# Kernel tuning notes

Measured on AMD Instinct MI355X. Metric: run time of the kernel, lower is better.

Reference implementation:

```python
import jax, jax.numpy as jnp
import numpy as np

B, N, D, H = 128, 197, 384, 1536  # batch, patches+CLS, embed_dim, hidden_dim


def _layer_norm(x, g, b, eps=1e-5):
    m = jnp.mean(x, axis=-1, keepdims=True)
    v = jnp.mean(jnp.square(x - m), axis=-1, keepdims=True)
    return (x - m) * jax.lax.rsqrt(v + eps) * g + b


def setup_inputs() -> dict:
    key = jax.random.key(0)
    ks = jax.random.split(key, 8)
    x = jax.random.normal(ks[0], (B, N, D), dtype=jnp.float32)
    # quantum circuit surrogates: orthogonal-style square matrices
    V = jax.random.normal(ks[1], (D, D), dtype=jnp.float32) / np.sqrt(D)
    W = jax.random.normal(ks[2], (D, D), dtype=jnp.float32) / np.sqrt(D)
    ln1_g = jnp.ones((D,), jnp.float32); ln1_b = jnp.zeros((D,), jnp.float32)
    ln2_g = jnp.ones((D,), jnp.float32); ln2_b = jnp.zeros((D,), jnp.float32)
    W1 = jax.random.normal(ks[3], (D, H), dtype=jnp.float32) / np.sqrt(D)
    b1 = jnp.zeros((H,), jnp.float32)
    W2 = jax.random.normal(ks[4], (H, D), dtype=jnp.float32) / np.sqrt(H)
    b2 = jnp.zeros((D,), jnp.float32)
    return {"x": x, "ln1_g": ln1_g, "ln1_b": ln1_b, "V": V, "W": W,
            "ln2_g": ln2_g, "ln2_b": ln2_b, "W1": W1, "b1": b1, "W2": W2, "b2": b2}


def reference(x, ln1_g, ln1_b, V, W, ln2_g, ln2_b, W1, b1, W2, b2):
    inp = _layer_norm(x, ln1_g, ln1_b)
    # normalization across the patch axis (dim=1), exactly as in the torch code
    inp = inp / jnp.sqrt(jnp.sum(jnp.square(inp) + 1e-4, axis=1, keepdims=True) + 1e-8)
    # Vx circuit: unary-basis probabilities |(V x_i)_d|^2 -> vx[b, d, i]
    vx = jnp.square(jnp.einsum('de,bne->bdn', V, inp))            # [B, D, N]
    # xWx circuit: (x_i^T W x_j)^2 -> xwx[b, i, j]
    y = jnp.einsum('bnd,de->bne', inp, W)                         # [B, N, D]
    xwx = jnp.square(jnp.einsum('bne,bme->bnm', y, inp))          # [B, N, N]
    vx = jnp.sqrt(vx + 1e-8)
    xwx = jnp.sqrt(xwx + 1e-8)
    attn = jax.nn.softmax(xwx, axis=-1)                           # [B, N, N]
    t = jnp.einsum('bnm,bdm->bnd', attn, vx)                      # attn @ vx^T
    x = x + t
    h = _layer_norm(x, ln2_g, ln2_b)
    h = jax.nn.gelu(h @ W1 + b1) @ W2 + b2                        # dropout=0 (eval)
    return x + h
```

## Files before the change

### kernel.cpp

```cpp
#include <hip/hip_runtime.h>
#include <math.h>

typedef unsigned short u16;
typedef unsigned int u32;
typedef __bf16 bfv8 __attribute__((ext_vector_type(8)));
typedef float f32x4 __attribute__((ext_vector_type(4)));

#define BB 128
#define NN 197
#define DD 384
#define HH 1536
#define BN (BB*NN)
#define NP 224

__device__ __forceinline__ u16 f2bf(float x){ u32 u; __builtin_memcpy(&u,&x,4); u = (u + 0x7fffu + ((u>>16)&1u))>>16; return (u16)u; }

__device__ __forceinline__ float fast_gelu(float z){
  float t2 = 1.5957691216f*z*(1.f + 0.044715f*z*z);
  return z * __builtin_amdgcn_rcpf(1.f + __expf(-t2));
}

__device__ __forceinline__ void gload16(const void* g, void* s){
  __builtin_amdgcn_global_load_lds(
      (const __attribute__((address_space(1))) void*)g,
      (__attribute__((address_space(3))) void*)s, 16, 0, 0);
}

__global__ __launch_bounds__(256) void ln1_stats(const float* __restrict__ x,
    float* __restrict__ mu, float* __restrict__ rv){
  int row = blockIdx.x*4 + (threadIdx.x>>6);
  int lane = threadIdx.x & 63;
  const float* xr = x + (long)row*DD;
  float s=0.f, ss=0.f;
  #pragma unroll
  for (int j=0;j<DD/64;j++){ float v = xr[lane + j*64]; s+=v; ss+=v*v; }
  #pragma unroll
  for (int m=32;m;m>>=1){ s += __shfl_xor(s,m); ss += __shfl_xor(ss,m); }
  if (lane==0){
    float mn = s*(1.f/DD);
    float var = ss*(1.f/DD) - mn*mn;
    mu[row]=mn; rv[row]=1.f/sqrtf(var+1e-5f);
  }
}

__global__ __launch_bounds__(256) void colnorm(const float* __restrict__ x,
    const float* __restrict__ mu, const float* __restrict__ rv,
    const float* __restrict__ g, const float* __restrict__ bt,
    float* __restrict__ scale){
  int i = blockIdx.x*256 + threadIdx.x;
  int b = i/DD, d = i - b*DD;
  const float* xp = x + (long)b*NN*DD + d;
  float gd = g[d], bd = bt[d];
  float s = 0.f;
  for (int n=0;n<NN;n++){
    float v = (xp[(long)n*DD] - mu[b*NN+n]) * rv[b*NN+n] * gd + bd;
    s += v*v;
  }
  scale[i] = 1.f/sqrtf(s + 197.f*1e-4f + 1e-8f);
}

__global__ __launch_bounds__(256) void ln_apply(const float* __restrict__ x,
    const float* __restrict__ mu, const float* __restrict__ rv,
    const float* __restrict__ g, const float* __restrict__ bt,
    const float* __restrict__ scale, u16* __restrict__ inpn){
  long i = (long)blockIdx.x*256 + threadIdx.x;
  int d = (int)(i % DD);
  long row = i / DD;
  int b = (int)(row / NN);
  float v = (x[i]-mu[row])*rv[row]*g[d]+bt[d];
  inpn[i] = f2bf(v * scale[b*DD+d]);
}

__global__ __launch_bounds__(256) void prep_weights(const float* __restrict__ V, const float* __restrict__ W,
    const float* __restrict__ W1, const float* __restrict__ W2,
    u16* __restrict__ Vb, u16* __restrict__ Wt, u16* __restrict__ W1t, u16* __restrict__ W2t){
  int i = blockIdx.x*256 + threadIdx.x;
  if (i < DD*DD){
    Vb[i] = f2bf(V[i]);
    int r = i/DD, c = i - r*DD;
    Wt[c*DD + r] = f2bf(W[i]);
  }
  {
    int r = i/HH, c = i - r*HH;
    W1t[(long)c*DD + r] = f2bf(W1[i]);
    int r2 = i/DD, c2 = i - r2*DD;
    W2t[(long)c2*HH + r2] = f2bf(W2[i]);
  }
}

__global__ __launch_bounds__(256) void softmax_rows(const float* __restrict__ S, u16* __restrict__ attn){
  int row = blockIdx.x*4 + (threadIdx.x>>6);
  int lane = threadIdx.x & 63;
  const float* sr = S + (long)row*NP;
  float v[4]; float mx = -1e30f;
  #pragma unroll
  for (int j=0;j<4;j++){ int c = lane + j*64; v[j] = (c<NN)? sr[c] : -1e30f; mx = fmaxf(mx, v[j]); }
  #pragma unroll
  for (int m=32;m;m>>=1) mx = fmaxf(mx, __shfl_xor(mx,m));
  float sm = 0.f;
  #pragma unroll
  for (int j=0;j<4;j++){ v[j] = __expf(v[j]-mx); sm += v[j]; }
  #pragma unroll
  for (int m=32;m;m>>=1) sm += __shfl_xor(sm,m);
  float inv = __builtin_amdgcn_rcpf(sm);
  u16* ar = attn + (long)row*NP;
  #pragma unroll
  for (int j=0;j<4;j++){ int c = lane + j*64; if (c<NP) ar[c] = f2bf(v[j]*inv); }
}

__global__ __launch_bounds__(256) void ln2_fused(const float* __restrict__ x2,
    const float* __restrict__ g, const float* __restrict__ bt, u16* __restrict__ h){
  int row = blockIdx.x*4 + (threadIdx.x>>6);
  int lane = threadIdx.x & 63;
  const float* xr = x2 + (long)row*DD;
  float v[6]; float s=0.f, ss=0.f;
  #pragma unroll
  for (int j=0;j<6;j++){ v[j]=xr[lane+j*64]; s+=v[j]; ss+=v[j]*v[j]; }
  #pragma unroll
  for (int m=32;m;m>>=1){ s+=__shfl_xor(s,m); ss+=__shfl_xor(ss,m); }
  float mn = s*(1.f/DD);
  float rvv = 1.f/sqrtf(ss*(1.f/DD)-mn*mn+1e-5f);
  u16* hr = h + (long)row*DD;
  #pragma unroll
  for (int j=0;j<6;j++){ int d = lane+j*64; hr[d] = f2bf((v[j]-mn)*rvv*g[d]+bt[d]); }
}

struct EpiUt { u16* ut;
  __device__ void operator()(int, int r0, int c, const f32x4* col) const {
    #pragma unroll
    for (int m=0;m<4;m++)
      #pragma unroll
      for (int i=0;i<4;i++){
        int r = r0 + m*16 + i;
        int b = r/NN, p = r - b*NN;
        float v = col[m][i];
        ut[((long)b*DD + c)*NP + p] = f2bf(sqrtf(v*v + 1e-8f));
      }
  }};
struct EpiY { u16* y;
  __device__ void operator()(int, int r0, int c, const f32x4* col) const {
    u16* yp = y + (long)r0*DD + c;
    #pragma unroll
    for (int m=0;m<4;m++)
      #pragma unroll
      for (int i=0;i<4;i++)
        yp[(long)(m*16+i)*DD] = f2bf(col[m][i]);
  }};
struct EpiS { float* s;
  __device__ void operator()(int b, int r0, int c, const f32x4* col) const {
    float* sp = s + ((long)b*NN + r0)*NP + c;
    #pragma unroll
    for (int m=0;m<4;m++)
      #pragma unroll
      for (int i=0;i<4;i++){
        int r = r0 + m*16 + i;
        float v = col[m][i];
        if (r < NN) sp[(long)(m*16+i)*NP] = sqrtf(v*v + 1e-8f);
      }
  }};
struct EpiX2 { float* x2; const float* x;
  __device__ void operator()(int b, int r0, int c, const f32x4* col) const {
    long base = ((long)b*NN + r0)*DD + c;
    #pragma unroll
    for (int m=0;m<4;m++)
      #pragma unroll
      for (int i=0;i<4;i++){
        int r = r0 + m*16 + i;
        if (r < NN){ long idx = base + (long)(m*16+i)*DD; x2[idx] = x[idx] + col[m][i]; }
      }
  }};
struct EpiGelu { u16* g; const float* b1;
  __device__ void operator()(int, int r0, int c, const f32x4* col) const {
    float bb = b1[c];
    u16* gp = g + (long)r0*HH + c;
    #pragma unroll
    for (int m=0;m<4;m++)
      #pragma unroll
      for (int i=0;i<4;i++)
        gp[(long)(m*16+i)*HH] = f2bf(fast_gelu(col[m][i] + bb));
  }};
struct EpiOut { float* o; const float* x2; const float* b2;
  __device__ void operator()(int, int r0, int c, const f32x4* col) const {
    float bb = b2[c];
    long base = (long)r0*DD + c;
    #pragma unroll
    for (int m=0;m<4;m++)
      #pragma unroll
      for (int i=0;i<4;i++){
        long idx = base + (long)(m*16+i)*DD;
        o[idx] = x2[idx] + col[m][i] + bb;
      }
  }};

template<class Epi>
__global__ __launch_bounds__(256) void gemm_nt(const u16* __restrict__ A, const u16* __restrict__ B,
    int M, int N, int K, int lda, int ldb, long sA, long sB, int NT, Epi epi)
{
  __shared__ __align__(16) u16 As[128*32];
  __shared__ __align__(16) u16 Bs[128*32];
  const int bm = blockIdx.x / NT, bn = blockIdx.x - bm*NT;
  const int bat = blockIdx.y;
  const u16* Ab = A + (long)bat*sA;
  const u16* Bb = B + (long)bat*sB;
  const int t = threadIdx.x, lane = t&63, wid = t>>6, wr = wid>>1, wc = wid&1;
  const int row0 = bm*128, col0 = bn*128;

  long aoff[2], boff[2]; int soff[2];
  #pragma unroll
  for (int i=0;i<2;i++){
    int ob = (i*256+t)*16;
    int r = ob>>6;
    int ke = (ob&63)>>1;
    int ra = row0+r; if (ra>M-1) ra=M-1;
    int rb = col0+r; if (rb>N-1) rb=N-1;
    aoff[i] = (long)ra*lda + ke;
    boff[i] = (long)rb*ldb + ke;
    soff[i] = ob;
  }

  f32x4 acc[4][4] = {};
  const int kg = (lane>>4)*8, rl = lane&15;

  for (int k0=0; k0<K; k0+=32){
    #pragma unroll
    for (int i=0;i<2;i++){
      gload16(Ab + aoff[i] + k0, (char*)As + soff[i]);
      gload16(Bb + boff[i] + k0, (char*)Bs + soff[i]);
    }
    __syncthreads();
    bfv8 af[4], bfr[4];
    #pragma unroll
    for (int m=0;m<4;m++) af[m]  = *(const bfv8*)&As[(wr*64 + m*16 + rl)*32 + kg];
    #pragma unroll
    for (int n=0;n<4;n++) bfr[n] = *(const bfv8*)&Bs[(wc*64 + n*16 + rl)*32 + kg];
    #pragma unroll
    for (int m=0;m<4;m++)
      #pragma unroll
      for (int n=0;n<4;n++)
        acc[m][n] = __builtin_amdgcn_mfma_f32_16x16x32_bf16(af[m], bfr[n], acc[m][n], 0,0,0);
    __syncthreads();
  }

  const int rbase = row0 + wr*64 + (lane>>4)*4;
  const int cbase = col0 + wc*64 + rl;
  #pragma unroll
  for (int n=0;n<4;n++){
    int c = cbase + n*16;
    if (c < N){
      f32x4 colv[4] = {acc[0][n], acc[1][n], acc[2][n], acc[3][n]};
      epi(bat, rbase, c, colv);
    }
  }
}

extern "C" void kernel_launch(void* const* d_in, const int* in_sizes, int n_in,
                              void* d_out, int out_size, void* d_ws, size_t ws_size,
                              hipStream_t stream){
  const float* x     = (const float*)d_in[0];
  const float* g1    = (const float*)d_in[1];
  const float* b1n   = (const float*)d_in[2];
  const float* V     = (const float*)d_in[3];
  const float* W     = (const float*)d_in[4];
  const float* g2    = (const float*)d_in[5];
  const float* b2n   = (const float*)d_in[6];
  const float* W1    = (const float*)d_in[7];
  const float* bias1 = (const float*)d_in[8];
  const float* W2    = (const float*)d_in[9];
  const float* bias2 = (const float*)d_in[10];
  float* out = (float*)d_out;

  char* ws = (char*)d_ws;
  size_t off = 0;
  auto take = [&](size_t bytes)->char*{ char* p = ws + off; off += (bytes + 255) & ~(size_t)255; return p; };

  float* mu    = (float*)take((size_t)BN*4);
  float* rv    = (float*)take((size_t)BN*4);
  float* scale = (float*)take((size_t)BB*DD*4);
  char* aliasBase = ws + off;
  u16*  inpn = (u16*) take((size_t)BN*DD*2);
  u16*  Ut   = (u16*) take((size_t)BB*DD*NP*2);
  u16*  Yb   = (u16*) take((size_t)BN*DD*2);
  float* S   = (float*)take((size_t)BN*NP*4);
  u16*  attn = (u16*) take((size_t)BN*NP*2);
  float* x2  = (float*)take((size_t)BN*DD*4);
  u16*  h    = (u16*) take((size_t)BN*DD*2);
  u16*  Vb   = (u16*) take((size_t)DD*DD*2);
  u16*  Wt   = (u16*) take((size_t)DD*DD*2);
  u16*  W1t  = (u16*) take((size_t)DD*HH*2);
  u16*  W2t  = (u16*) take((size_t)DD*HH*2);
  u16*  G    = (u16*)aliasBase;

  prep_weights<<<DD*HH/256, 256, 0, stream>>>(V, W, W1, W2, Vb, Wt, W1t, W2t);
  ln1_stats  <<<BN/4,       256, 0, stream>>>(x, mu, rv);
  colnorm    <<<BB*DD/256,  256, 0, stream>>>(x, mu, rv, g1, b1n, scale);
  ln_apply   <<<BN*DD/256,  256, 0, stream>>>(x, mu, rv, g1, b1n, scale, inpn);
  (void)hipMemsetAsync(Ut, 0, (size_t)BB*DD*NP*2, stream);

  { dim3 grid(197*3, 1);
    gemm_nt<EpiUt><<<grid,256,0,stream>>>(inpn, Vb, BN, DD, DD, DD, DD, 0, 0, 3, EpiUt{Ut}); }
  { dim3 grid(197*3, 1);
    gemm_nt<EpiY><<<grid,256,0,stream>>>(inpn, Wt, BN, DD, DD, DD, DD, 0, 0, 3, EpiY{Yb}); }
  { dim3 grid(4, BB);
    gemm_nt<EpiS><<<grid,256,0,stream>>>(Yb, inpn, NN, NN, DD, DD, DD,
                                         (long)NN*DD, (long)NN*DD, 2, EpiS{S}); }
  softmax_rows<<<BN/4, 256, 0, stream>>>(S, attn);
  { dim3 grid(6, BB);
    gemm_nt<EpiX2><<<grid,256,0,stream>>>(attn, Ut, NN, DD, NP, NP, NP,
                                          (long)NN*NP, (long)DD*NP, 3, EpiX2{x2, x}); }
  ln2_fused<<<BN/4, 256, 0, stream>>>(x2, g2, b2n, h);
  { dim3 grid(197*12, 1);
    gemm_nt<EpiGelu><<<grid,256,0,stream>>>(h, W1t, BN, HH, DD, DD, DD, 0, 0, 12, EpiGelu{G, bias1}); }
  { dim3 grid(197*3, 1);
    gemm_nt<EpiOut><<<grid,256,0,stream>>>(G, W2t, BN, DD, HH, HH, HH, 0, 0, 3, EpiOut{out, x2, bias2}); }
}
```

Baseline: 442.0 us.

## Fuse LN1 stats, column norm and apply into one per-batch kernel; XCD-aware GEMM tile remap

```diff
diff --git a/kernel.cpp b/kernel.cpp
--- a/kernel.cpp
+++ b/kernel.cpp
@@ -26,49 +26,39 @@
       (__attribute__((address_space(3))) void*)s, 16, 0, 0);
 }
 
-__global__ __launch_bounds__(256) void ln1_stats(const float* __restrict__ x,
-    float* __restrict__ mu, float* __restrict__ rv){
-  int row = blockIdx.x*4 + (threadIdx.x>>6);
-  int lane = threadIdx.x & 63;
-  const float* xr = x + (long)row*DD;
-  float s=0.f, ss=0.f;
-  #pragma unroll
-  for (int j=0;j<DD/64;j++){ float v = xr[lane + j*64]; s+=v; ss+=v*v; }
-  #pragma unroll
-  for (int m=32;m;m>>=1){ s += __shfl_xor(s,m); ss += __shfl_xor(ss,m); }
-  if (lane==0){
-    float mn = s*(1.f/DD);
-    float var = ss*(1.f/DD) - mn*mn;
-    mu[row]=mn; rv[row]=1.f/sqrtf(var+1e-5f);
-  }
-}
-
-__global__ __launch_bounds__(256) void colnorm(const float* __restrict__ x,
-    const float* __restrict__ mu, const float* __restrict__ rv,
-    const float* __restrict__ g, const float* __restrict__ bt,
-    float* __restrict__ scale){
-  int i = blockIdx.x*256 + threadIdx.x;
-  int b = i/DD, d = i - b*DD;
-  const float* xp = x + (long)b*NN*DD + d;
-  float gd = g[d], bd = bt[d];
-  float s = 0.f;
-  for (int n=0;n<NN;n++){
-    float v = (xp[(long)n*DD] - mu[b*NN+n]) * rv[b*NN+n] * gd + bd;
-    s += v*v;
-  }
-  scale[i] = 1.f/sqrtf(s + 197.f*1e-4f + 1e-8f);
-}
-
-__global__ __launch_bounds__(256) void ln_apply(const float* __restrict__ x,
-    const float* __restrict__ mu, const float* __restrict__ rv,
-    const float* __restrict__ g, const float* __restrict__ bt,
-    const float* __restrict__ scale, u16* __restrict__ inpn){
-  long i = (long)blockIdx.x*256 + threadIdx.x;
-  int d = (int)(i % DD);
-  long row = i / DD;
-  int b = (int)(row / NN);
-  float v = (x[i]-mu[row])*rv[row]*g[d]+bt[d];
-  inpn[i] = f2bf(v * scale[b*DD+d]);
+__global__ __launch_bounds__(512) void ln1_colnorm_apply(const float* __restrict__ x,
+    const float* __restrict__ g, const float* __restrict__ bt, u16* __restrict__ inpn){
+  __shared__ float smu[NN], srv[NN], sscale[DD];
+  const int b = blockIdx.x;
+  const float* xb = x + (long)b*NN*DD;
+  u16* ob = inpn + (long)b*NN*DD;
+  const int t = threadIdx.x, lane = t&63, wid = t>>6;
+  for (int r = wid; r < NN; r += 8){
+    const float* xr = xb + (long)r*DD;
+    float s=0.f, ss=0.f;
+    #pragma unroll
+    for (int j=0;j<6;j++){ float v = xr[lane+j*64]; s+=v; ss+=v*v; }
+    #pragma unroll
+    for (int m=32;m;m>>=1){ s+=__shfl_xor(s,m); ss+=__shfl_xor(ss,m); }
+    if (lane==0){ float mn=s*(1.f/DD); smu[r]=mn; srv[r]=1.f/sqrtf(ss*(1.f/DD)-mn*mn+1e-5f); }
+  }
+  __syncthreads();
+  if (t < DD){
+    float gd=g[t], bd=bt[t];
+    float s=0.f;
+    #pragma unroll 4
+    for (int n=0;n<NN;n++){
+      float v=(xb[(long)n*DD+t]-smu[n])*srv[n]*gd+bd;
+      s += v*v;
+    }
+    sscale[t]=1.f/sqrtf(s + 197.f*1e-4f + 1e-8f);
+  }
+  __syncthreads();
+  for (int i=t; i<NN*DD; i+=512){
+    int n = i/DD, d = i-n*DD;
+    float v=(xb[i]-smu[n])*srv[n]*g[d]+bt[d];
+    ob[i]=f2bf(v*sscale[d]);
+  }
 }
 
 __global__ __launch_bounds__(256) void prep_weights(const float* __restrict__ V, const float* __restrict__ W,
@@ -198,7 +188,12 @@
 {
   __shared__ __align__(16) u16 As[128*32];
   __shared__ __align__(16) u16 Bs[128*32];
-  const int bm = blockIdx.x / NT, bn = blockIdx.x - bm*NT;
+  int wg;
+  { int flat = blockIdx.x, nwg = gridDim.x;
+    int xcd = flat & 7, local = flat >> 3;
+    int q = nwg >> 3, r = nwg & 7;
+    wg = (xcd < r ? xcd*(q+1) : r*(q+1) + (xcd-r)*q) + local; }
+  const int bm = wg / NT, bn = wg - bm*NT;
   const int bat = blockIdx.y;
   const u16* Ab = A + (long)bat*sA;
   const u16* Bb = B + (long)bat*sB;
@@ -273,10 +268,7 @@
   size_t off = 0;
   auto take = [&](size_t bytes)->char*{ char* p = ws + off; off += (bytes + 255) & ~(size_t)255; return p; };
 
-  float* mu    = (float*)take((size_t)BN*4);
-  float* rv    = (float*)take((size_t)BN*4);
-  float* scale = (float*)take((size_t)BB*DD*4);
-  char* aliasBase = ws + off;
+  char* aliasBase = ws;
   u16*  inpn = (u16*) take((size_t)BN*DD*2);
   u16*  Ut   = (u16*) take((size_t)BB*DD*NP*2);
   u16*  Yb   = (u16*) take((size_t)BN*DD*2);
@@ -291,9 +283,7 @@
   u16*  G    = (u16*)aliasBase;
 
   prep_weights<<<DD*HH/256, 256, 0, stream>>>(V, W, W1, W2, Vb, Wt, W1t, W2t);
-  ln1_stats  <<<BN/4,       256, 0, stream>>>(x, mu, rv);
-  colnorm    <<<BB*DD/256,  256, 0, stream>>>(x, mu, rv, g1, b1n, scale);
-  ln_apply   <<<BN*DD/256,  256, 0, stream>>>(x, mu, rv, g1, b1n, scale, inpn);
+  ln1_colnorm_apply<<<BB, 512, 0, stream>>>(x, g1, b1n, inpn);
   (void)hipMemsetAsync(Ut, 0, (size_t)BB*DD*NP*2, stream);
 
   { dim3 grid(197*3, 1);
```

Result: slower. 458.1 us (+3.7%).
